# Kernel optimization log

Hardware: AMD Instinct MI355X
Metric: run time of the kernel (lower is better)

The kernel has to match this reference:

```python
import jax, jax.numpy as jnp
import numpy as np

H, D = 8, 16
NA, NB, E, F = 50000, 50000, 200000, 128
SQRT_D = float(np.sqrt(D))


def _proj(x, W, b):
    # Linear then split heads: [N, F] -> [N, H, D]
    return (x @ W + b).reshape(x.shape[0], H, D)


def _seg_softmax(alpha, idx, n):
    # softmax over edges sharing the same destination node (per head)
    amax = jax.ops.segment_max(alpha, idx, num_segments=n)
    amax = jnp.where(jnp.isfinite(amax), amax, 0.0)
    ex = jnp.exp(alpha - amax[idx])
    den = jax.ops.segment_sum(ex, idx, num_segments=n)
    return ex / (den[idx] + 1e-16)


def _hgt_conv(xa, xb, eis, Wk, bk, Wq, bq, Wv, bv, Wa, ba, skip, arel, mrel, prel):
    # node types: 0='a', 1='b'; edge types: 0 a->b, 1 b->a, 2 a->a
    xs = (xa, xb)
    k = [_proj(xs[t], Wk[t], bk[t]) for t in range(2)]
    q = [_proj(xs[t], Wq[t], bq[t]) for t in range(2)]
    v = [_proj(xs[t], Wv[t], bv[t]) for t in range(2)]
    nn_ = (xa.shape[0], xb.shape[0])
    agg = [jnp.zeros((nn_[t], H, D), xa.dtype) for t in range(2)]
    spec = ((0, 1, eis[0]), (1, 0, eis[1]), (0, 0, eis[2]))
    for e, (s, d, ei) in enumerate(spec):
        src, dst = ei[0], ei[1]
        k_rel = jnp.einsum('nhd,hde->nhe', k[s], arel[e])  # [Ns,H,D]
        v_rel = jnp.einsum('nhd,hde->nhe', v[s], mrel[e])
        alpha = jnp.sum(q[d][dst] * k_rel[src], axis=-1) * prel[e] / SQRT_D  # [E,H]
        w = _seg_softmax(alpha, dst, nn_[d])
        agg[d] = agg[d] + jax.ops.segment_sum(v_rel[src] * w[..., None], dst, num_segments=nn_[d])
    outs = []
    for t in range(2):
        o = jax.nn.gelu(agg[t].reshape(-1, H * D), approximate=False) @ Wa[t] + ba[t]
        sgate = jax.nn.sigmoid(skip[t])  # learned skip-gate, dims match so always applied
        outs.append(sgate * o + (1.0 - sgate) * xs[t])
    return outs[0], outs[1]


def _forward(xa, xb, eis, Wk, bk, Wq, bq, Wv, bv, Wa, ba, skip, arel, mrel, prel):
    for l in range(2):
        xa, xb = _hgt_conv(xa, xb, eis, Wk[l], bk[l], Wq[l], bq[l], Wv[l], bv[l],
                           Wa[l], ba[l], skip[l], arel[l], mrel[l], prel[l])
        if l < 1:
            xa, xb = jax.nn.relu(xa), jax.nn.relu(xb)  # dropout: identity in eval mode
    return xa, xb


def setup_inputs() -> dict:
    key = jax.random.key(0)
    ks = jax.random.split(key, 12)
    s = 0.05
    return {
        'xa': jax.random.normal(ks[0], (NA, F), jnp.float32),
        'xb': jax.random.normal(ks[1], (NB, F), jnp.float32),
        'ei_ab': jax.random.randint(ks[2], (2, E), 0, NA, dtype=jnp.int32),
        'ei_ba': jax.random.randint(ks[3], (2, E), 0, NB, dtype=jnp.int32),
        'ei_aa': jax.random.randint(ks[4], (2, E), 0, NA, dtype=jnp.int32),
        'Wk': jax.random.normal(ks[5], (2, 2, F, F), jnp.float32) * s,
        'bk': jnp.zeros((2, 2, F), jnp.float32),
        'Wq': jax.random.normal(ks[6], (2, 2, F, F), jnp.float32) * s,
        'bq': jnp.zeros((2, 2, F), jnp.float32),
        'Wv': jax.random.normal(ks[7], (2, 2, F, F), jnp.float32) * s,
        'bv': jnp.zeros((2, 2, F), jnp.float32),
        'Wa': jax.random.normal(ks[8], (2, 2, F, F), jnp.float32) * s,
        'ba': jnp.zeros((2, 2, F), jnp.float32),
        'skip': jnp.zeros((2, 2), jnp.float32),
        'arel': jax.random.normal(ks[9], (2, 3, H, D, D), jnp.float32) * (1.0 / SQRT_D),
        'mrel': jax.random.normal(ks[10], (2, 3, H, D, D), jnp.float32) * (1.0 / SQRT_D),
        'prel': jnp.ones((2, 3, H), jnp.float32),
    }


def reference(xa, xb, ei_ab, ei_ba, ei_aa, Wk, bk, Wq, bq, Wv, bv, Wa, ba, skip, arel, mrel, prel):
    return _forward(xa, xb, (ei_ab, ei_ba, ei_aa), Wk, bk, Wq, bq, Wv, bv, Wa, ba, skip, arel, mrel, prel)
```

## Files before the change

### kernel.cpp

```cpp
#include <hip/hip_runtime.h>
#include <hip/hip_bf16.h>
#include <math.h>

#define F 128
#define NH 8
#define HD 16

static inline int cdiv(int a, int b) { return (a + b - 1) / b; }

typedef __attribute__((ext_vector_type(8))) short bf16x8;
typedef __attribute__((ext_vector_type(4))) float f32x4;

__device__ __forceinline__ float geluf(float x) {
    return 0.5f * x * (1.f + erff(x * 0.70710678118654752440f));
}

__device__ __forceinline__ short f2bf(float f) {
    __hip_bfloat16 h = __float2bfloat16(f);
    return *reinterpret_cast<short*>(&h);
}

__device__ __forceinline__ float bflo(unsigned int u) { return __uint_as_float(u << 16); }
__device__ __forceinline__ float bfhi(unsigned int u) { return __uint_as_float(u & 0xffff0000u); }
__device__ __forceinline__ float bf2f(short s) {
    return __uint_as_float(((unsigned int)(unsigned short)s) << 16);
}
__device__ __forceinline__ unsigned int packbf(float a, float b) {
    return (unsigned int)(unsigned short)f2bf(a) | ((unsigned int)(unsigned short)f2bf(b) << 16);
}

__device__ __forceinline__ void glds16(const void* g, void* l) {
    __builtin_amdgcn_global_load_lds(
        (const __attribute__((address_space(1))) unsigned int*)g,
        (__attribute__((address_space(3))) unsigned int*)l, 16, 0, 0);
}

__device__ __forceinline__ void slot_info(int slot, int& kind, int& wsel, int& e, int& t) {
    switch (slot) {
        case 0: kind = 0; wsel = 0; t = 0; e = 0; break;
        case 1: kind = 1; wsel = 1; t = 0; e = 0; break;
        case 2: kind = 1; wsel = 2; t = 0; e = 0; break;
        case 3: kind = 1; wsel = 1; t = 0; e = 2; break;
        case 4: kind = 1; wsel = 2; t = 0; e = 2; break;
        case 5: kind = 0; wsel = 0; t = 1; e = 0; break;
        case 6: kind = 1; wsel = 1; t = 1; e = 1; break;
        case 7: kind = 1; wsel = 2; t = 1; e = 1; break;
        case 8: kind = 0; wsel = 3; t = 0; e = 0; break;
        default: kind = 0; wsel = 3; t = 1; e = 0; break;
    }
}

__global__ void prep_weights(const float* __restrict__ Wk, const float* __restrict__ bk,
                             const float* __restrict__ Wq, const float* __restrict__ bq,
                             const float* __restrict__ Wv, const float* __restrict__ bv,
                             const float* __restrict__ Wa, const float* __restrict__ ba,
                             const float* __restrict__ arel, const float* __restrict__ mrel,
                             short* __restrict__ Wslots, float* __restrict__ bslots) {
    const int WTOT = 10 * 16384;
    const int layer = blockIdx.y;
    short* Wl = Wslots + (size_t)layer * WTOT;
    float* bl = bslots + (size_t)layer * 10 * 128;
    int idx = blockIdx.x * blockDim.x + threadIdx.x;
    if (idx < WTOT) {
        int slot = idx >> 14, rem = idx & 16383;
        int n = rem >> 7, k = rem & 127;
        int kind, wsel, e, t;
        slot_info(slot, kind, wsel, e, t);
        float out;
        if (kind == 0) {
            const float* Wb = (wsel == 0 ? Wq : Wa) + (size_t)(layer * 2 + t) * 16384;
            out = Wb[k * 128 + n];
        } else {
            int h = n >> 4, j = n & 15;
            const float* Wb = (wsel == 1 ? Wk : Wv) + (size_t)(layer * 2 + t) * 16384;
            const float* R = (wsel == 1 ? arel : mrel) + (size_t)((layer * 3 + e) * NH + h) * 256;
            float s = 0.f;
            #pragma unroll
            for (int d = 0; d < HD; ++d) s += Wb[k * 128 + h * 16 + d] * R[d * 16 + j];
            out = s;
        }
        int chunk = k >> 3, kin = k & 7;
        int cph = (chunk + (n & 15)) & 15;
        Wl[(size_t)slot * 16384 + n * 128 + cph * 8 + kin] = f2bf(out);
    } else {
        int r = idx - WTOT;
        if (r < 10 * 128) {
            int slot = r >> 7, n = r & 127;
            int kind, wsel, e, t;
            slot_info(slot, kind, wsel, e, t);
            float out;
            if (kind == 0) {
                const float* bb = (wsel == 0 ? bq : ba) + (size_t)(layer * 2 + t) * 128;
                out = bb[n];
            } else {
                int h = n >> 4, j = n & 15;
                const float* bb = (wsel == 1 ? bk : bv) + (size_t)(layer * 2 + t) * 128;
                const float* R = (wsel == 1 ? arel : mrel) + (size_t)((layer * 3 + e) * NH + h) * 256;
                float s = 0.f;
                #pragma unroll
                for (int d = 0; d < HD; ++d) s += bb[h * 16 + d] * R[d * 16 + j];
                out = s;
            }
            bl[slot * 128 + n] = out;
        }
    }
}

__device__ __forceinline__ short* qkv_slot_ptr(int side, int s,
    short* qA, short* kA0, short* vA0, short* kA2, short* vA2,
    short* qB, short* kB1, short* vB1) {
    if (side) {
        if (s == 0) return qB;
        if (s == 1) return kB1;
        return vB1;
    }
    if (s == 0) return qA;
    if (s == 1) return kA0;
    if (s == 2) return vA0;
    if (s == 3) return kA2;
    return vA2;
}

__device__ __forceinline__ void stage_W(const short* __restrict__ Wt, short* Ws,
                                        int wave, int lane) {
    #pragma unroll
    for (int it = 0; it < 8; ++it) {
        int off = (it * 4 + wave) * 1024;
        glds16((const char*)Wt + off + lane * 16, (char*)Ws + off);
    }
}

__global__ __launch_bounds__(256) void gemm_qkv_all(
    const float* __restrict__ Aa, const float* __restrict__ Ab,
    const short* __restrict__ Wl, const float* __restrict__ bl,
    short* __restrict__ qA, short* __restrict__ kA0, short* __restrict__ vA0,
    short* __restrict__ kA2, short* __restrict__ vA2,
    short* __restrict__ qB, short* __restrict__ kB1, short* __restrict__ vB1,
    int NA_, int NB_, int nbA) {
    __shared__ __align__(16) float Wsf[64 * 132];
    __shared__ __align__(16) short As[64 * 136];
    short* Ws = (short*)Wsf;
    const int tid = threadIdx.x;
    const int bid = blockIdx.x;
    const int side = bid >= nbA;
    const float* A = side ? Ab : Aa;
    const int N = side ? NB_ : NA_;
    const int row0 = (side ? bid - nbA : bid) * 64;
    const short* Wbase = Wl + (side ? (size_t)5 * 16384 : 0);
    const float* bbase = bl + (side ? 5 * 128 : 0);
    const int S = side ? 3 : 5;

    const int wave = tid >> 6;
    const int lane = tid & 63;
    const int m16 = lane & 15;
    const int kg = lane >> 4;
    const int arow = wave * 16 + m16;

    #pragma unroll
    for (int it = 0; it < 4; ++it) {
        int chunk = tid + it * 256;
        int r = chunk >> 4, c8 = (chunk & 15) * 8;
        int gr = row0 + r;
        bf16x8 s = {};
        if (gr < N) {
            float4 v0 = *(const float4*)&A[(size_t)gr * F + c8];
            float4 v1 = *(const float4*)&A[(size_t)gr * F + c8 + 4];
            s[0] = f2bf(v0.x); s[1] = f2bf(v0.y); s[2] = f2bf(v0.z); s[3] = f2bf(v0.w);
            s[4] = f2bf(v1.x); s[5] = f2bf(v1.y); s[6] = f2bf(v1.z); s[7] = f2bf(v1.w);
        }
        *(bf16x8*)&As[r * 136 + c8] = s;
    }
    __syncthreads();

    bf16x8 af[4];
    #pragma unroll
    for (int kq = 0; kq < 4; ++kq)
        af[kq] = *(const bf16x8*)&As[arow * 136 + kq * 32 + kg * 8];

    for (int s = 0; s < S; ++s) {
        if (s) __syncthreads();
        stage_W(Wbase + (size_t)s * 16384, Ws, wave, lane);
        __syncthreads();

        f32x4 acc[8] = {};
        #pragma unroll
        for (int kq = 0; kq < 4; ++kq) {
            #pragma unroll
            for (int nt = 0; nt < 8; ++nt) {
                int cph = (kq * 4 + kg + m16) & 15;
                bf16x8 b = *(const bf16x8*)&Ws[(nt * 16 + m16) * 128 + cph * 8];
                acc[nt] = __builtin_amdgcn_mfma_f32_16x16x32_bf16(af[kq], b, acc[nt], 0, 0, 0);
            }
        }
        __syncthreads();

        #pragma unroll
        for (int nt = 0; nt < 8; ++nt)
            #pragma unroll
            for (int r = 0; r < 4; ++r)
                Wsf[(wave * 16 + kg * 4 + r) * 132 + nt * 16 + m16] = acc[nt][r];
        __syncthreads();

        short* optr = qkv_slot_ptr(side, s, qA, kA0, vA0, kA2, vA2, qB, kB1, vB1);
        const float* bias = bbase + s * 128;
        #pragma unroll
        for (int it = 0; it < 4; ++it) {
            int chunk = tid + it * 256;
            int r = chunk >> 4, c8 = (chunk & 15) * 8;
            int gr = row0 + r;
            if (gr >= N) continue;
            float4 b0 = *(const float4*)&bias[c8];
            float4 b1 = *(const float4*)&bias[c8 + 4];
            float4 va = *(float4*)&Wsf[r * 132 + c8];
            float4 vb = *(float4*)&Wsf[r * 132 + c8 + 4];
            bf16x8 o;
            o[0] = f2bf(va.x + b0.x); o[1] = f2bf(va.y + b0.y);
            o[2] = f2bf(va.z + b0.z); o[3] = f2bf(va.w + b0.w);
            o[4] = f2bf(vb.x + b1.x); o[5] = f2bf(vb.y + b1.y);
            o[6] = f2bf(vb.z + b1.z); o[7] = f2bf(vb.w + b1.w);
            *(bf16x8*)&optr[(size_t)gr * F + c8] = o;
        }
    }
}

__global__ __launch_bounds__(256) void fused_out_qkv(
    const short* __restrict__ aggA, const short* __restrict__ aggB,
    const short* __restrict__ Wl0, const float* __restrict__ bl0,
    const float* __restrict__ xfA, const float* __restrict__ xfB,
    const float* __restrict__ skipp,
    const short* __restrict__ Wl1, const float* __restrict__ bl1,
    short* __restrict__ x1A, short* __restrict__ x1B,
    short* __restrict__ qA, short* __restrict__ kA0, short* __restrict__ vA0,
    short* __restrict__ kA2, short* __restrict__ vA2,
    short* __restrict__ qB, short* __restrict__ kB1, short* __restrict__ vB1,
    int NA_, int NB_, int nbA) {
    __shared__ __align__(16) float Wsf[64 * 132];
    __shared__ __align__(16) short As[64 * 136];
    short* Ws = (short*)Wsf;
    const int tid = threadIdx.x;
    const int bid = blockIdx.x;
    const int side = bid >= nbA;
    const short* A = side ? aggB : aggA;
    const int N = side ? NB_ : NA_;
    const int row0 = (side ? bid - nbA : bid) * 64;
    const short* Wt0 = Wl0 + (size_t)(side ? 9 : 8) * 16384;
    const float* bias0 = bl0 + (side ? 9 : 8) * 128;

    const int wave = tid >> 6;
    const int lane = tid & 63;
    const int m16 = lane & 15;
    const int kg = lane >> 4;
    const int arow = wave * 16 + m16;

    stage_W(Wt0, Ws, wave, lane);
    #pragma unroll
    for (int it = 0; it < 4; ++it) {
        int chunk = tid + it * 256;
        int r = chunk >> 4, c8 = (chunk & 15) * 8;
        int gr = row0 + r;
        bf16x8 s = {};
        if (gr < N) {
            s = *(const bf16x8*)&A[(size_t)gr * F + c8];
            #pragma unroll
            for (int u = 0; u < 8; ++u) s[u] = f2bf(geluf(bf2f(s[u])));
        }
        *(bf16x8*)&As[r * 136 + c8] = s;
    }
    __syncthreads();

    {
        f32x4 acc[8] = {};
        #pragma unroll
        for (int kq = 0; kq < 4; ++kq) {
            bf16x8 a = *(const bf16x8*)&As[arow * 136 + kq * 32 + kg * 8];
            #pragma unroll
            for (int nt = 0; nt < 8; ++nt) {
                int cph = (kq * 4 + kg + m16) & 15;
                bf16x8 b = *(const bf16x8*)&Ws[(nt * 16 + m16) * 128 + cph * 8];
                acc[nt] = __builtin_amdgcn_mfma_f32_16x16x32_bf16(a, b, acc[nt], 0, 0, 0);
            }
        }
        __syncthreads();
        #pragma unroll
        for (int nt = 0; nt < 8; ++nt)
            #pragma unroll
            for (int r = 0; r < 4; ++r)
                Wsf[(wave * 16 + kg * 4 + r) * 132 + nt * 16 + m16] = acc[nt][r];
        __syncthreads();
    }

    {
        float sg = 1.f / (1.f + expf(-skipp[side]));
        short* x1 = side ? x1B : x1A;
        const float* xf = side ? xfB : xfA;
        #pragma unroll
        for (int it = 0; it < 4; ++it) {
            int chunk = tid + it * 256;
            int r = chunk >> 4, c8 = (chunk & 15) * 8;
            int gr = row0 + r;
            if (gr >= N) continue;
            float4 b0 = *(const float4*)&bias0[c8];
            float4 b1 = *(const float4*)&bias0[c8 + 4];
            float4 va = *(float4*)&Wsf[r * 132 + c8];
            float4 vb = *(float4*)&Wsf[r * 132 + c8 + 4];
            float4 x0v = *(const float4*)&xf[(size_t)gr * F + c8];
            float4 x1v = *(const float4*)&xf[(size_t)gr * F + c8 + 4];
            float v[8] = {va.x + b0.x, va.y + b0.y, va.z + b0.z, va.w + b0.w,
                          vb.x + b1.x, vb.y + b1.y, vb.z + b1.z, vb.w + b1.w};
            float xr[8] = {x0v.x, x0v.y, x0v.z, x0v.w, x1v.x, x1v.y, x1v.z, x1v.w};
            bf16x8 o;
            #pragma unroll
            for (int u = 0; u < 8; ++u)
                o[u] = f2bf(fmaxf(sg * v[u] + (1.f - sg) * xr[u], 0.f));
            *(bf16x8*)&x1[(size_t)gr * F + c8] = o;
            *(bf16x8*)&As[r * 136 + c8] = o;
        }
    }
    __syncthreads();

    bf16x8 af[4];
    #pragma unroll
    for (int kq = 0; kq < 4; ++kq)
        af[kq] = *(const bf16x8*)&As[arow * 136 + kq * 32 + kg * 8];

    const short* Wbase = Wl1 + (side ? (size_t)5 * 16384 : 0);
    const float* bbase = bl1 + (side ? 5 * 128 : 0);
    const int S = side ? 3 : 5;

    for (int s = 0; s < S; ++s) {
        __syncthreads();
        stage_W(Wbase + (size_t)s * 16384, Ws, wave, lane);
        __syncthreads();

        f32x4 acc[8] = {};
        #pragma unroll
        for (int kq = 0; kq < 4; ++kq) {
            #pragma unroll
            for (int nt = 0; nt < 8; ++nt) {
                int cph = (kq * 4 + kg + m16) & 15;
                bf16x8 b = *(const bf16x8*)&Ws[(nt * 16 + m16) * 128 + cph * 8];
                acc[nt] = __builtin_amdgcn_mfma_f32_16x16x32_bf16(af[kq], b, acc[nt], 0, 0, 0);
            }
        }
        __syncthreads();

        #pragma unroll
        for (int nt = 0; nt < 8; ++nt)
            #pragma unroll
            for (int r = 0; r < 4; ++r)
                Wsf[(wave * 16 + kg * 4 + r) * 132 + nt * 16 + m16] = acc[nt][r];
        __syncthreads();

        short* optr = qkv_slot_ptr(side, s, qA, kA0, vA0, kA2, vA2, qB, kB1, vB1);
        const float* bias = bbase + s * 128;
        #pragma unroll
        for (int it = 0; it < 4; ++it) {
            int chunk = tid + it * 256;
            int r = chunk >> 4, c8 = (chunk & 15) * 8;
            int gr = row0 + r;
            if (gr >= N) continue;
            float4 b0 = *(const float4*)&bias[c8];
            float4 b1 = *(const float4*)&bias[c8 + 4];
            float4 va = *(float4*)&Wsf[r * 132 + c8];
            float4 vb = *(float4*)&Wsf[r * 132 + c8 + 4];
            bf16x8 o;
            o[0] = f2bf(va.x + b0.x); o[1] = f2bf(va.y + b0.y);
            o[2] = f2bf(va.z + b0.z); o[3] = f2bf(va.w + b0.w);
            o[4] = f2bf(vb.x + b1.x); o[5] = f2bf(vb.y + b1.y);
            o[6] = f2bf(vb.z + b1.z); o[7] = f2bf(vb.w + b1.w);
            *(bf16x8*)&optr[(size_t)gr * F + c8] = o;
        }
    }
}

__global__ __launch_bounds__(256) void gemm_out_final(
    const short* __restrict__ aggA, const short* __restrict__ aggB,
    const short* __restrict__ Wl, const float* __restrict__ bl,
    const short* __restrict__ xbA, const short* __restrict__ xbB,
    const float* __restrict__ skipp,
    float* __restrict__ CfA, float* __restrict__ CfB,
    int NA_, int NB_, int nbA) {
    __shared__ __align__(16) float Wsf[64 * 132];
    __shared__ __align__(16) short As[64 * 136];
    short* Ws = (short*)Wsf;
    const int tid = threadIdx.x;
    const int bid = blockIdx.x;
    const int side = bid >= nbA;
    const short* A = side ? aggB : aggA;
    const int N = side ? NB_ : NA_;
    const int row0 = (side ? bid - nbA : bid) * 64;
    const short* Wt = Wl + (size_t)(side ? 9 : 8) * 16384;
    const float* bias = bl + (side ? 9 : 8) * 128;

    const int wave = tid >> 6;
    const int lane = tid & 63;
    const int m16 = lane & 15;
    const int kg = lane >> 4;
    const int arow = wave * 16 + m16;

    stage_W(Wt, Ws, wave, lane);
    #pragma unroll
    for (int it = 0; it < 4; ++it) {
        int chunk = tid + it * 256;
        int r = chunk >> 4, c8 = (chunk & 15) * 8;
        int gr = row0 + r;
        bf16x8 s = {};
        if (gr < N) {
            s = *(const bf16x8*)&A[(size_t)gr * F + c8];
            #pragma unroll
            for (int u = 0; u < 8; ++u) s[u] = f2bf(geluf(bf2f(s[u])));
        }
        *(bf16x8*)&As[r * 136 + c8] = s;
    }
    __syncthreads();

    f32x4 acc[8] = {};
    #pragma unroll
    for (int kq = 0; kq < 4; ++kq) {
        bf16x8 a = *(const bf16x8*)&As[arow * 136 + kq * 32 + kg * 8];
        #pragma unroll
        for (int nt = 0; nt < 8; ++nt) {
            int cph = (kq * 4 + kg + m16) & 15;
            bf16x8 b = *(const bf16x8*)&Ws[(nt * 16 + m16) * 128 + cph * 8];
            acc[nt] = __builtin_amdgcn_mfma_f32_16x16x32_bf16(a, b, acc[nt], 0, 0, 0);
        }
    }
    __syncthreads();

    #pragma unroll
    for (int nt = 0; nt < 8; ++nt)
        #pragma unroll
        for (int r = 0; r < 4; ++r)
            Wsf[(wave * 16 + kg * 4 + r) * 132 + nt * 16 + m16] = acc[nt][r];
    __syncthreads();

    float sg = 1.f / (1.f + expf(-skipp[side]));
    #pragma unroll
    for (int it = 0; it < 4; ++it) {
        int chunk = tid + it * 256;
        int r = chunk >> 4, c8 = (chunk & 15) * 8;
        int gr = row0 + r;
        if (gr >= N) continue;
        float4 b0 = *(const float4*)&bias[c8];
        float4 b1 = *(const float4*)&bias[c8 + 4];
        float4 va = *(float4*)&Wsf[r * 132 + c8];
        float4 vb = *(float4*)&Wsf[r * 132 + c8 + 4];
        float v[8] = {va.x + b0.x, va.y + b0.y, va.z + b0.z, va.w + b0.w,
                      vb.x + b1.x, vb.y + b1.y, vb.z + b1.z, vb.w + b1.w};
        const short* xb = side ? xbB : xbA;
        bf16x8 xrv = *(const bf16x8*)&xb[(size_t)gr * F + c8];
        float* Cf = side ? CfB : CfA;
        float o[8];
        #pragma unroll
        for (int u = 0; u < 8; ++u)
            o[u] = sg * v[u] + (1.f - sg) * bf2f(xrv[u]);
        *(float4*)&Cf[(size_t)gr * F + c8]     = make_float4(o[0], o[1], o[2], o[3]);
        *(float4*)&Cf[(size_t)gr * F + c8 + 4] = make_float4(o[4], o[5], o[6], o[7]);
    }
}


__global__ void hist_all(const int* __restrict__ ei0, const int* __restrict__ ei1,
                         const int* __restrict__ ei2, int E0, int E1, int E2,
                         int NB_, int NA_, int* __restrict__ cnt) {
    int i = blockIdx.x * 256 + threadIdx.x;
    if (i >= E0 + E1 + E2) return;
    const int* ei; int li, Ee, base;
    if (i < E0)           { li = i;           ei = ei0; Ee = E0; base = 0; }
    else if (i < E0 + E1) { li = i - E0;      ei = ei1; Ee = E1; base = NB_; }
    else                  { li = i - E0 - E1; ei = ei2; Ee = E2; base = NB_ + NA_; }
    atomicAdd(&cnt[base + ei[Ee + li]], 1);
}

__global__ void scan1(const int* __restrict__ cnt, int n, int* __restrict__ off,
                      int* __restrict__ bsum) {
    __shared__ int lds[256];
    int tid = threadIdx.x, i = blockIdx.x * 256 + tid;
    int v = (i < n) ? cnt[i] : 0;
    lds[tid] = v;
    __syncthreads();
    #pragma unroll
    for (int s = 1; s < 256; s <<= 1) {
        int t = (tid >= s) ? lds[tid - s] : 0;
        __syncthreads();
        lds[tid] += t;
        __syncthreads();
    }
    if (i < n) off[i] = lds[tid] - v;
    if (tid == 255) bsum[blockIdx.x] = lds[255];
}

__global__ __launch_bounds__(1024) void scan2(int* __restrict__ bsum, int nb,
                                              int* __restrict__ off_n) {
    __shared__ int lds[1024];
    int tid = threadIdx.x;
    int v = (tid < nb) ? bsum[tid] : 0;
    lds[tid] = v;
    __syncthreads();
    #pragma unroll
    for (int s = 1; s < 1024; s <<= 1) {
        int t = (tid >= s) ? lds[tid - s] : 0;
        __syncthreads();
        lds[tid] += t;
        __syncthreads();
    }
    if (tid < nb) bsum[tid] = lds[tid] - v;
    if (tid == 1023) *off_n = lds[1023];
}

__global__ void scan3(int* __restrict__ off, int* __restrict__ woff,
                      const int* __restrict__ bsum, int n) {
    int i = blockIdx.x * 256 + threadIdx.x;
    if (i < n) {
        int v = off[i] + bsum[blockIdx.x];
        off[i] = v;
        woff[i] = v;
    }
}

__global__ void scatter_all(const int* __restrict__ ei0, const int* __restrict__ ei1,
                            const int* __restrict__ ei2, int E0, int E1, int E2,
                            int NB_, int NA_, int* __restrict__ woff,
                            int* __restrict__ csr_src) {
    int i = blockIdx.x * 256 + threadIdx.x;
    if (i >= E0 + E1 + E2) return;
    const int* ei; int li, Ee, base;
    if (i < E0)           { li = i;           ei = ei0; Ee = E0; base = 0; }
    else if (i < E0 + E1) { li = i - E0;      ei = ei1; Ee = E1; base = NB_; }
    else                  { li = i - E0 - E1; ei = ei2; Ee = E2; base = NB_ + NA_; }
    int p = atomicAdd(&woff[base + ei[Ee + li]], 1);
    csr_src[p] = ei[li] * 16;
}

__device__ __forceinline__ void seg_set4(
    const uint4* __restrict__ kArr, const uint4* __restrict__ vArr,
    int c0, int e1, const int* __restrict__ csr, int s, int p,
    const float* __restrict__ qf, float pr,
    float* __restrict__ accv, float& den) {
    for (; c0 < e1; c0 += 4) {
        int rem = e1 - c0;
        bool act = s < rem;
        int sj = csr[c0 + (act ? s : 0)];
        uint4 kw = kArr[sj + p];
        uint4 vw = vArr[sj + p];
        float d = bflo(kw.x) * qf[0];
        d = fmaf(bfhi(kw.x), qf[1], d);
        d = fmaf(bflo(kw.y), qf[2], d);
        d = fmaf(bfhi(kw.y), qf[3], d);
        d = fmaf(bflo(kw.z), qf[4], d);
        d = fmaf(bfhi(kw.z), qf[5], d);
        d = fmaf(bflo(kw.w), qf[6], d);
        d = fmaf(bfhi(kw.w), qf[7], d);
        d += __shfl_xor(d, 1);
        float ex = __expf(fminf(d * pr, 80.f));
        ex = act ? ex : 0.f;
        den += ex;
        accv[0] = fmaf(ex, bflo(vw.x), accv[0]);
        accv[1] = fmaf(ex, bfhi(vw.x), accv[1]);
        accv[2] = fmaf(ex, bflo(vw.y), accv[2]);
        accv[3] = fmaf(ex, bfhi(vw.y), accv[3]);
        accv[4] = fmaf(ex, bflo(vw.z), accv[4]);
        accv[5] = fmaf(ex, bfhi(vw.z), accv[5]);
        accv[6] = fmaf(ex, bflo(vw.w), accv[6]);
        accv[7] = fmaf(ex, bfhi(vw.w), accv[7]);
    }
}

__device__ __forceinline__ void seg_fold(float* __restrict__ accv, float& den,
                                         float* __restrict__ r) {
    #pragma unroll
    for (int j = 0; j < 8; ++j) {
        accv[j] += __shfl_xor(accv[j], 16);
        accv[j] += __shfl_xor(accv[j], 32);
    }
    den += __shfl_xor(den, 16);
    den += __shfl_xor(den, 32);
    float inv = 1.f / (den + 1e-16f);
    #pragma unroll
    for (int j = 0; j < 8; ++j) r[j] = fmaf(accv[j], inv, r[j]);
}

__global__ __launch_bounds__(256) void seg_attn_all(
    const short* __restrict__ qA, const short* __restrict__ kA0,
    const short* __restrict__ vA0, const short* __restrict__ kA2,
    const short* __restrict__ vA2, const short* __restrict__ qB,
    const short* __restrict__ kB1, const short* __restrict__ vB1,
    const int* __restrict__ off0, const int* __restrict__ off1,
    const int* __restrict__ off2, const int* __restrict__ csrS,
    const float* __restrict__ prelL,
    short* __restrict__ aggA, short* __restrict__ aggB,
    int NA_, int NB_, int nba) {
    const int wv = threadIdx.x >> 6;
    const int l = threadIdx.x & 63;
    const int s = l >> 4;
    const int p = l & 15;
    const int h = p >> 1;
    const int isA = (int)blockIdx.x < nba;
    int dst = (isA ? blockIdx.x : blockIdx.x - nba) * 4 + wv;
    if (dst >= (isA ? NA_ : NB_)) return;

    uint4 qw = ((const uint4*)(isA ? qA : qB))[(size_t)dst * 16 + p];
    float qf[8] = {bflo(qw.x), bfhi(qw.x), bflo(qw.y), bfhi(qw.y),
                   bflo(qw.z), bfhi(qw.z), bflo(qw.w), bfhi(qw.w)};

    float r[8] = {};
    float accv[8] = {};
    float den = 0.f;
    if (isA) {
        seg_set4((const uint4*)kB1, (const uint4*)vB1, off1[dst], off1[dst + 1],
                 csrS, s, p, qf, prelL[1 * NH + h] * 0.25f, accv, den);
        seg_fold(accv, den, r);
        #pragma unroll
        for (int j = 0; j < 8; ++j) accv[j] = 0.f;
        den = 0.f;
        seg_set4((const uint4*)kA2, (const uint4*)vA2, off2[dst], off2[dst + 1],
                 csrS, s, p, qf, prelL[2 * NH + h] * 0.25f, accv, den);
        seg_fold(accv, den, r);
    } else {
        seg_set4((const uint4*)kA0, (const uint4*)vA0, off0[dst], off0[dst + 1],
                 csrS, s, p, qf, prelL[0 * NH + h] * 0.25f, accv, den);
        seg_fold(accv, den, r);
    }
    if (s == 0) {
        uint4 o;
        o.x = packbf(r[0], r[1]);
        o.y = packbf(r[2], r[3]);
        o.z = packbf(r[4], r[5]);
        o.w = packbf(r[6], r[7]);
        ((uint4*)(isA ? aggA : aggB))[(size_t)dst * 16 + p] = o;
    }
}

extern "C" void kernel_launch(void* const* d_in, const int* in_sizes, int n_in,
                              void* d_out, int out_size, void* d_ws, size_t ws_size,
                              hipStream_t stream) {
    const float* xa   = (const float*)d_in[0];
    const float* xb   = (const float*)d_in[1];
    const int* ei_ab  = (const int*)d_in[2];
    const int* ei_ba  = (const int*)d_in[3];
    const int* ei_aa  = (const int*)d_in[4];
    const float* Wk   = (const float*)d_in[5];
    const float* bk   = (const float*)d_in[6];
    const float* Wq   = (const float*)d_in[7];
    const float* bq   = (const float*)d_in[8];
    const float* Wv   = (const float*)d_in[9];
    const float* bv   = (const float*)d_in[10];
    const float* Wa   = (const float*)d_in[11];
    const float* ba   = (const float*)d_in[12];
    const float* skip = (const float*)d_in[13];
    const float* arel = (const float*)d_in[14];
    const float* mrel = (const float*)d_in[15];
    const float* prel = (const float*)d_in[16];

    const int NA = in_sizes[0] / F;
    const int NB = in_sizes[1] / F;
    const int E0 = in_sizes[2] / 2, E1 = in_sizes[3] / 2, E2 = in_sizes[4] / 2;
    const int ET = E0 + E1 + E2;
    const int NT = NB + NA + NA;

    float* ws = (float*)d_ws;
    size_t o = 0;
    float* bslots = ws + o; o += 2 * 10 * 128;
    int* iws = (int*)(ws + o);
    size_t io = 0;
    int* cnt   = iws + io; io += NT;
    int* bsum  = iws + io; io += 1024;
    int* offc  = iws + io; io += NT + 1;
    int* woff  = iws + io; io += NT;
    int* csrS  = iws + io; io += ET;
    io = (io + 7) & ~(size_t)7;
    short* sws = (short*)(iws + io);
    size_t so = 0;
    short* qA  = sws + so; so += (size_t)NA * 128;
    short* kA0 = sws + so; so += (size_t)NA * 128;
    short* vA0 = sws + so; so += (size_t)NA * 128;
    short* kA2 = sws + so; so += (size_t)NA * 128;
    short* vA2 = sws + so; so += (size_t)NA * 128;
    short* qB  = sws + so; so += (size_t)NB * 128;
    short* kB1 = sws + so; so += (size_t)NB * 128;
    short* vB1 = sws + so; so += (size_t)NB * 128;
    short* aggA = sws + so; so += (size_t)NA * 128;
    short* aggB = sws + so; so += (size_t)NB * 128;
    short* x1ab = sws + so; so += (size_t)NA * 128;
    short* x1bb = sws + so; so += (size_t)NB * 128;
    short* Wslots = sws + so; so += (size_t)2 * 10 * 16384;

    float* outA = (float*)d_out;
    float* outB = (float*)d_out + (size_t)NA * F;

    {
        dim3 g(cdiv(10 * 16384 + 10 * 128, 256), 2);
        prep_weights<<<g, 256, 0, stream>>>(Wk, bk, Wq, bq, Wv, bv, Wa, ba,
                                            arel, mrel, Wslots, bslots);
    }

    hipMemsetAsync(cnt, 0, (size_t)NT * sizeof(int), stream);
    hist_all<<<cdiv(ET, 256), 256, 0, stream>>>(ei_ab, ei_ba, ei_aa, E0, E1, E2, NB, NA, cnt);
    {
        int nb = cdiv(NT, 256);
        scan1<<<nb, 256, 0, stream>>>(cnt, NT, offc, bsum);
        scan2<<<1, 1024, 0, stream>>>(bsum, nb, offc + NT);
        scan3<<<nb, 256, 0, stream>>>(offc, woff, bsum, NT);
    }
    scatter_all<<<cdiv(ET, 256), 256, 0, stream>>>(ei_ab, ei_ba, ei_aa, E0, E1, E2, NB, NA, woff, csrS);

    const int* off_e0 = offc;
    const int* off_e1 = offc + NB;
    const int* off_e2 = offc + NB + NA;

    const int nbA64 = cdiv(NA, 64), nbB64 = cdiv(NB, 64);
    const int nba4 = cdiv(NA, 4), nbb4 = cdiv(NB, 4);

    const short* Wl0 = Wslots;
    const short* Wl1 = Wslots + (size_t)10 * 16384;
    const float* bl0 = bslots;
    const float* bl1 = bslots + 10 * 128;

    gemm_qkv_all<<<nbA64 + nbB64, 256, 0, stream>>>(
        xa, xb, Wl0, bl0, qA, kA0, vA0, kA2, vA2, qB, kB1, vB1, NA, NB, nbA64);

    seg_attn_all<<<nba4 + nbb4, 256, 0, stream>>>(
        qA, kA0, vA0, kA2, vA2, qB, kB1, vB1,
        off_e0, off_e1, off_e2, csrS, prel, aggA, aggB, NA, NB, nba4);

    fused_out_qkv<<<nbA64 + nbB64, 256, 0, stream>>>(
        aggA, aggB, Wl0, bl0, xa, xb, skip, Wl1, bl1,
        x1ab, x1bb, qA, kA0, vA0, kA2, vA2, qB, kB1, vB1, NA, NB, nbA64);

    seg_attn_all<<<nba4 + nbb4, 256, 0, stream>>>(
        qA, kA0, vA0, kA2, vA2, qB, kB1, vB1,
        off_e0, off_e1, off_e2, csrS, prel + 3 * NH, aggA, aggB, NA, NB, nba4);

    gemm_out_final<<<nbA64 + nbB64, 256, 0, stream>>>(
        aggA, aggB, Wl1, bl1, x1ab, x1bb, skip + 2, outA, outB, NA, NB, nbA64);
}
```

Before: 335.7 us.

## Merge weight prep, input bf16 conversion and histogram into one launch; fuse scan1 into GEMM

Weight preparation, a new fp32-to-bf16 conversion of the node features, and the edge histogram now run as block ranges of a single kernel. The first scan pass is appended as extra blocks of the QKV GEMM launch. The GEMM and the layer-1 skip path then read bf16 features instead of fp32. This cuts kernel launches and serialization and halves feature read traffic in the GEMMs, at the cost of an extra conversion pass and bf16 rounding of the skip-connection input.

```diff
diff --git a/kernel.cpp b/kernel.cpp
--- a/kernel.cpp
+++ b/kernel.cpp
@@ -50,59 +50,93 @@
     }
 }
 
-__global__ void prep_weights(const float* __restrict__ Wk, const float* __restrict__ bk,
-                             const float* __restrict__ Wq, const float* __restrict__ bq,
-                             const float* __restrict__ Wv, const float* __restrict__ bv,
-                             const float* __restrict__ Wa, const float* __restrict__ ba,
-                             const float* __restrict__ arel, const float* __restrict__ mrel,
-                             short* __restrict__ Wslots, float* __restrict__ bslots) {
+__global__ void prep_all(const float* __restrict__ Wk, const float* __restrict__ bk,
+                         const float* __restrict__ Wq, const float* __restrict__ bq,
+                         const float* __restrict__ Wv, const float* __restrict__ bv,
+                         const float* __restrict__ Wa, const float* __restrict__ ba,
+                         const float* __restrict__ arel, const float* __restrict__ mrel,
+                         const float* __restrict__ xa, const float* __restrict__ xb,
+                         const int* __restrict__ ei0, const int* __restrict__ ei1,
+                         const int* __restrict__ ei2,
+                         short* __restrict__ Wslots, float* __restrict__ bslots,
+                         short* __restrict__ xab, short* __restrict__ xbb,
+                         int* __restrict__ cnt,
+                         int NA_, int NB_, int E0, int E1, int E2,
+                         int PWB, int CONVB) {
     const int WTOT = 10 * 16384;
-    const int layer = blockIdx.y;
-    short* Wl = Wslots + (size_t)layer * WTOT;
-    float* bl = bslots + (size_t)layer * 10 * 128;
-    int idx = blockIdx.x * blockDim.x + threadIdx.x;
-    if (idx < WTOT) {
-        int slot = idx >> 14, rem = idx & 16383;
-        int n = rem >> 7, k = rem & 127;
-        int kind, wsel, e, t;
-        slot_info(slot, kind, wsel, e, t);
-        float out;
-        if (kind == 0) {
-            const float* Wb = (wsel == 0 ? Wq : Wa) + (size_t)(layer * 2 + t) * 16384;
-            out = Wb[k * 128 + n];
-        } else {
-            int h = n >> 4, j = n & 15;
-            const float* Wb = (wsel == 1 ? Wk : Wv) + (size_t)(layer * 2 + t) * 16384;
-            const float* R = (wsel == 1 ? arel : mrel) + (size_t)((layer * 3 + e) * NH + h) * 256;
-            float s = 0.f;
-            #pragma unroll
-            for (int d = 0; d < HD; ++d) s += Wb[k * 128 + h * 16 + d] * R[d * 16 + j];
-            out = s;
-        }
-        int chunk = k >> 3, kin = k & 7;
-        int cph = (chunk + (n & 15)) & 15;
-        Wl[(size_t)slot * 16384 + n * 128 + cph * 8 + kin] = f2bf(out);
-    } else {
-        int r = idx - WTOT;
-        if (r < 10 * 128) {
-            int slot = r >> 7, n = r & 127;
+    const int bid = blockIdx.x;
+    const int tid = threadIdx.x;
+    if (bid < 2 * PWB) {
+        const int layer = bid / PWB;
+        short* Wl = Wslots + (size_t)layer * WTOT;
+        float* bl = bslots + (size_t)layer * 10 * 128;
+        int idx = (bid % PWB) * 256 + tid;
+        if (idx < WTOT) {
+            int slot = idx >> 14, rem = idx & 16383;
+            int n = rem >> 7, k = rem & 127;
             int kind, wsel, e, t;
             slot_info(slot, kind, wsel, e, t);
             float out;
             if (kind == 0) {
-                const float* bb = (wsel == 0 ? bq : ba) + (size_t)(layer * 2 + t) * 128;
-                out = bb[n];
+                const float* Wb = (wsel == 0 ? Wq : Wa) + (size_t)(layer * 2 + t) * 16384;
+                out = Wb[k * 128 + n];
             } else {
                 int h = n >> 4, j = n & 15;
-                const float* bb = (wsel == 1 ? bk : bv) + (size_t)(layer * 2 + t) * 128;
+                const float* Wb = (wsel == 1 ? Wk : Wv) + (size_t)(layer * 2 + t) * 16384;
                 const float* R = (wsel == 1 ? arel : mrel) + (size_t)((layer * 3 + e) * NH + h) * 256;
                 float s = 0.f;
                 #pragma unroll
-                for (int d = 0; d < HD; ++d) s += bb[h * 16 + d] * R[d * 16 + j];
+                for (int d = 0; d < HD; ++d) s += Wb[k * 128 + h * 16 + d] * R[d * 16 + j];
                 out = s;
             }
-            bl[slot * 128 + n] = out;
-        }
+            int chunk = k >> 3, kin = k & 7;
+            int cph = (chunk + (n & 15)) & 15;
+            Wl[(size_t)slot * 16384 + n * 128 + cph * 8 + kin] = f2bf(out);
+        } else {
+            int r = idx - WTOT;
+            if (r < 10 * 128) {
+                int slot = r >> 7, n = r & 127;
+                int kind, wsel, e, t;
+                slot_info(slot, kind, wsel, e, t);
+                float out;
+                if (kind == 0) {
+                    const float* bb = (wsel == 0 ? bq : ba) + (size_t)(layer * 2 + t) * 128;
+                    out = bb[n];
+                } else {
+                    int h = n >> 4, j = n & 15;
+                    const float* bb = (wsel == 1 ? bk : bv) + (size_t)(layer * 2 + t) * 128;
+                    const float* R = (wsel == 1 ? arel : mrel) + (size_t)((layer * 3 + e) * NH + h) * 256;
+                    float s = 0.f;
+                    #pragma unroll
+                    for (int d = 0; d < HD; ++d) s += bb[h * 16 + d] * R[d * 16 + j];
+                    out = s;
+                }
+                bl[slot * 128 + n] = out;
+            }
+        }
+    } else if (bid < 2 * PWB + CONVB) {
+        int gi = (bid - 2 * PWB) * 256 + tid;
+        int total8 = (NA_ + NB_) * 16;
+        if (gi < total8) {
+            size_t e = (size_t)gi * 8;
+            const float* src; short* dst; size_t off;
+            if (e < (size_t)NA_ * 128) { src = xa; dst = xab; off = e; }
+            else { src = xb; dst = xbb; off = e - (size_t)NA_ * 128; }
+            float4 v0 = *(const float4*)&src[off];
+            float4 v1 = *(const float4*)&src[off + 4];
+            bf16x8 s;
+            s[0] = f2bf(v0.x); s[1] = f2bf(v0.y); s[2] = f2bf(v0.z); s[3] = f2bf(v0.w);
+            s[4] = f2bf(v1.x); s[5] = f2bf(v1.y); s[6] = f2bf(v1.z); s[7] = f2bf(v1.w);
+            *(bf16x8*)&dst[off] = s;
+        }
+    } else {
+        int i = (bid - 2 * PWB - CONVB) * 256 + tid;
+        if (i >= E0 + E1 + E2) return;
+        const int* ei; int li, Ee, base;
+        if (i < E0)           { li = i;           ei = ei0; Ee = E0; base = 0; }
+        else if (i < E0 + E1) { li = i - E0;      ei = ei1; Ee = E1; base = NB_; }
+        else                  { li = i - E0 - E1; ei = ei2; Ee = E2; base = NB_ + NA_; }
+        atomicAdd(&cnt[base + ei[Ee + li]], 1);
     }
 }
 
@@ -131,19 +165,40 @@
 }
 
 __global__ __launch_bounds__(256) void gemm_qkv_all(
-    const float* __restrict__ Aa, const float* __restrict__ Ab,
+    const short* __restrict__ Aa, const short* __restrict__ Ab,
     const short* __restrict__ Wl, const float* __restrict__ bl,
     short* __restrict__ qA, short* __restrict__ kA0, short* __restrict__ vA0,
     short* __restrict__ kA2, short* __restrict__ vA2,
     short* __restrict__ qB, short* __restrict__ kB1, short* __restrict__ vB1,
-    int NA_, int NB_, int nbA) {
+    int NA_, int NB_, int nbA, int nbGemm,
+    const int* __restrict__ cnt, int* __restrict__ offc, int* __restrict__ bsum, int NT) {
     __shared__ __align__(16) float Wsf[64 * 132];
     __shared__ __align__(16) short As[64 * 136];
+    __shared__ int slds[256];
     short* Ws = (short*)Wsf;
     const int tid = threadIdx.x;
     const int bid = blockIdx.x;
+
+    if (bid >= nbGemm) {
+        int blk = bid - nbGemm;
+        int i = blk * 256 + tid;
+        int v = (i < NT) ? cnt[i] : 0;
+        slds[tid] = v;
+        __syncthreads();
+        #pragma unroll
+        for (int s = 1; s < 256; s <<= 1) {
+            int t = (tid >= s) ? slds[tid - s] : 0;
+            __syncthreads();
+            slds[tid] += t;
+            __syncthreads();
+        }
+        if (i < NT) offc[i] = slds[tid] - v;
+        if (tid == 255) bsum[blk] = slds[255];
+        return;
+    }
+
     const int side = bid >= nbA;
-    const float* A = side ? Ab : Aa;
+    const short* A = side ? Ab : Aa;
     const int N = side ? NB_ : NA_;
     const int row0 = (side ? bid - nbA : bid) * 64;
     const short* Wbase = Wl + (side ? (size_t)5 * 16384 : 0);
@@ -162,12 +217,7 @@
         int r = chunk >> 4, c8 = (chunk & 15) * 8;
         int gr = row0 + r;
         bf16x8 s = {};
-        if (gr < N) {
-            float4 v0 = *(const float4*)&A[(size_t)gr * F + c8];
-            float4 v1 = *(const float4*)&A[(size_t)gr * F + c8 + 4];
-            s[0] = f2bf(v0.x); s[1] = f2bf(v0.y); s[2] = f2bf(v0.z); s[3] = f2bf(v0.w);
-            s[4] = f2bf(v1.x); s[5] = f2bf(v1.y); s[6] = f2bf(v1.z); s[7] = f2bf(v1.w);
-        }
+        if (gr < N) s = *(const bf16x8*)&A[(size_t)gr * F + c8];
         *(bf16x8*)&As[r * 136 + c8] = s;
     }
     __syncthreads();
@@ -226,7 +276,7 @@
 __global__ __launch_bounds__(256) void fused_out_qkv(
     const short* __restrict__ aggA, const short* __restrict__ aggB,
     const short* __restrict__ Wl0, const float* __restrict__ bl0,
-    const float* __restrict__ xfA, const float* __restrict__ xfB,
+    const short* __restrict__ xabA, const short* __restrict__ xabB,
     const float* __restrict__ skipp,
     const short* __restrict__ Wl1, const float* __restrict__ bl1,
     short* __restrict__ x1A, short* __restrict__ x1B,
@@ -292,7 +342,7 @@
     {
         float sg = 1.f / (1.f + expf(-skipp[side]));
         short* x1 = side ? x1B : x1A;
-        const float* xf = side ? xfB : xfA;
+        const short* xf = side ? xabB : xabA;
         #pragma unroll
         for (int it = 0; it < 4; ++it) {
             int chunk = tid + it * 256;
@@ -303,15 +353,13 @@
             float4 b1 = *(const float4*)&bias0[c8 + 4];
             float4 va = *(float4*)&Wsf[r * 132 + c8];
             float4 vb = *(float4*)&Wsf[r * 132 + c8 + 4];
-            float4 x0v = *(const float4*)&xf[(size_t)gr * F + c8];
-            float4 x1v = *(const float4*)&xf[(size_t)gr * F + c8 + 4];
+            bf16x8 xrv = *(const bf16x8*)&xf[(size_t)gr * F + c8];
             float v[8] = {va.x + b0.x, va.y + b0.y, va.z + b0.z, va.w + b0.w,
                           vb.x + b1.x, vb.y + b1.y, vb.z + b1.z, vb.w + b1.w};
-            float xr[8] = {x0v.x, x0v.y, x0v.z, x0v.w, x1v.x, x1v.y, x1v.z, x1v.w};
             bf16x8 o;
             #pragma unroll
             for (int u = 0; u < 8; ++u)
-                o[u] = f2bf(fmaxf(sg * v[u] + (1.f - sg) * xr[u], 0.f));
+                o[u] = f2bf(fmaxf(sg * v[u] + (1.f - sg) * bf2f(xrv[u]), 0.f));
             *(bf16x8*)&x1[(size_t)gr * F + c8] = o;
             *(bf16x8*)&As[r * 136 + c8] = o;
         }
@@ -459,36 +507,6 @@
     }
 }
 
-
-__global__ void hist_all(const int* __restrict__ ei0, const int* __restrict__ ei1,
-                         const int* __restrict__ ei2, int E0, int E1, int E2,
-                         int NB_, int NA_, int* __restrict__ cnt) {
-    int i = blockIdx.x * 256 + threadIdx.x;
-    if (i >= E0 + E1 + E2) return;
-    const int* ei; int li, Ee, base;
-    if (i < E0)           { li = i;           ei = ei0; Ee = E0; base = 0; }
-    else if (i < E0 + E1) { li = i - E0;      ei = ei1; Ee = E1; base = NB_; }
-    else                  { li = i - E0 - E1; ei = ei2; Ee = E2; base = NB_ + NA_; }
-    atomicAdd(&cnt[base + ei[Ee + li]], 1);
-}
-
-__global__ void scan1(const int* __restrict__ cnt, int n, int* __restrict__ off,
-                      int* __restrict__ bsum) {
-    __shared__ int lds[256];
-    int tid = threadIdx.x, i = blockIdx.x * 256 + tid;
-    int v = (i < n) ? cnt[i] : 0;
-    lds[tid] = v;
-    __syncthreads();
-    #pragma unroll
-    for (int s = 1; s < 256; s <<= 1) {
-        int t = (tid >= s) ? lds[tid - s] : 0;
-        __syncthreads();
-        lds[tid] += t;
-        __syncthreads();
-    }
-    if (i < n) off[i] = lds[tid] - v;
-    if (tid == 255) bsum[blockIdx.x] = lds[255];
-}
 
 __global__ __launch_bounds__(1024) void scan2(int* __restrict__ bsum, int nb,
                                               int* __restrict__ off_n) {
@@ -683,32 +701,19 @@
     short* aggB = sws + so; so += (size_t)NB * 128;
     short* x1ab = sws + so; so += (size_t)NA * 128;
     short* x1bb = sws + so; so += (size_t)NB * 128;
+    short* xab  = sws + so; so += (size_t)NA * 128;
+    short* xbb  = sws + so; so += (size_t)NB * 128;
     short* Wslots = sws + so; so += (size_t)2 * 10 * 16384;
 
     float* outA = (float*)d_out;
     float* outB = (float*)d_out + (size_t)NA * F;
 
-    {
-        dim3 g(cdiv(10 * 16384 + 10 * 128, 256), 2);
-        prep_weights<<<g, 256, 0, stream>>>(Wk, bk, Wq, bq, Wv, bv, Wa, ba,
-                                            arel, mrel, Wslots, bslots);
-    }
-
-    hipMemsetAsync(cnt, 0, (size_t)NT * sizeof(int), stream);
-    hist_all<<<cdiv(ET, 256), 256, 0, stream>>>(ei_ab, ei_ba, ei_aa, E0, E1, E2, NB, NA, cnt);
-    {
-        int nb = cdiv(NT, 256);
-        scan1<<<nb, 256, 0, stream>>>(cnt, NT, offc, bsum);
-        scan2<<<1, 1024, 0, stream>>>(bsum, nb, offc + NT);
-        scan3<<<nb, 256, 0, stream>>>(offc, woff, bsum, NT);
-    }
-    scatter_all<<<cdiv(ET, 256), 256, 0, stream>>>(ei_ab, ei_ba, ei_aa, E0, E1, E2, NB, NA, woff, csrS);
-
-    const int* off_e0 = offc;
-    const int* off_e1 = offc + NB;
-    const int* off_e2 = offc + NB + NA;
-
+    const int PWB = cdiv(10 * 16384 + 10 * 128, 256);
+    const int CONVB = cdiv((NA + NB) * 16, 256);
+    const int HISTB = cdiv(ET, 256);
     const int nbA64 = cdiv(NA, 64), nbB64 = cdiv(NB, 64);
+    const int nbGemm = nbA64 + nbB64;
+    const int nbScan = cdiv(NT, 256);
     const int nba4 = cdiv(NA, 4), nbb4 = cdiv(NB, 4);
 
     const short* Wl0 = Wslots;
@@ -716,15 +721,31 @@
     const float* bl0 = bslots;
     const float* bl1 = bslots + 10 * 128;
 
-    gemm_qkv_all<<<nbA64 + nbB64, 256, 0, stream>>>(
-        xa, xb, Wl0, bl0, qA, kA0, vA0, kA2, vA2, qB, kB1, vB1, NA, NB, nbA64);
+    hipMemsetAsync(cnt, 0, (size_t)NT * sizeof(int), stream);
+
+    prep_all<<<2 * PWB + CONVB + HISTB, 256, 0, stream>>>(
+        Wk, bk, Wq, bq, Wv, bv, Wa, ba, arel, mrel, xa, xb,
+        ei_ab, ei_ba, ei_aa, Wslots, bslots, xab, xbb, cnt,
+        NA, NB, E0, E1, E2, PWB, CONVB);
+
+    gemm_qkv_all<<<nbGemm + nbScan, 256, 0, stream>>>(
+        xab, xbb, Wl0, bl0, qA, kA0, vA0, kA2, vA2, qB, kB1, vB1,
+        NA, NB, nbA64, nbGemm, cnt, offc, bsum, NT);
+
+    scan2<<<1, 1024, 0, stream>>>(bsum, nbScan, offc + NT);
+    scan3<<<nbScan, 256, 0, stream>>>(offc, woff, bsum, NT);
+    scatter_all<<<HISTB, 256, 0, stream>>>(ei_ab, ei_ba, ei_aa, E0, E1, E2, NB, NA, woff, csrS);
+
+    const int* off_e0 = offc;
+    const int* off_e1 = offc + NB;
+    const int* off_e2 = offc + NB + NA;
 
     seg_attn_all<<<nba4 + nbb4, 256, 0, stream>>>(
         qA, kA0, vA0, kA2, vA2, qB, kB1, vB1,
         off_e0, off_e1, off_e2, csrS, prel, aggA, aggB, NA, NB, nba4);
 
     fused_out_qkv<<<nbA64 + nbB64, 256, 0, stream>>>(
-        aggA, aggB, Wl0, bl0, xa, xb, skip, Wl1, bl1,
+        aggA, aggB, Wl0, bl0, xab, xbb, skip, Wl1, bl1,
         x1ab, x1bb, qA, kA0, vA0, kA2, vA2, qB, kB1, vB1, NA, NB, nbA64);
 
     seg_attn_all<<<nba4 + nbb4, 256, 0, stream>>>(
```

Result: no change. 340.0 us (+1.3%).
